# Kernel tuning notes

Hardware: AMD Instinct MI355X
Metric: run time of the kernel (lower is better)

## Reference

```python
import jax, jax.numpy as jnp
import numpy as np

B, S, H, I, E = 2, 2048, 2048, 1408, 8
TOP_K = 2


def setup_inputs() -> dict:
    key = jax.random.key(0)
    k0, k1, k2, k3, k4 = jax.random.split(key, 5)
    scale = float(np.sqrt(2.0 / (H + I)))
    return {
        "hidden_states": jax.random.normal(k0, (B, S, H), dtype=jnp.float32),
        "router_w": jax.random.normal(k1, (E, H), dtype=jnp.float32) * (H ** -0.5),
        "gate_w": jax.random.normal(k2, (E, I, H), dtype=jnp.float32) * scale,
        "up_w": jax.random.normal(k3, (E, I, H), dtype=jnp.float32) * scale,
        "down_w": jax.random.normal(k4, (E, H, I), dtype=jnp.float32) * scale,
    }


def reference(hidden_states, router_w, gate_w, up_w, down_w):
    b, s, h = hidden_states.shape
    e = router_w.shape[0]
    x = hidden_states.reshape(-1, h)  # [T, H]

    # Router: top-k logits, softmax over the selected logits.
    logits = jnp.einsum("th,eh->te", x, router_w)          # [T, E]
    top_vals, top_idx = jax.lax.top_k(logits, TOP_K)        # [T, K]
    top_w = jax.nn.softmax(top_vals, axis=-1)               # [T, K]
    # The original module only uses the top-1 expert and its weight.
    expert = top_idx[:, 0]                                  # [T] int
    weight = top_w[:, 0]                                    # [T]

    # Per-expert gated MLP applied densely, then combined with a one-hot
    # top-1 dispatch mask scaled by the routing weight (same math as the
    # gather -> grouped GEMM -> weighted scatter in the original).
    gate = jnp.einsum("th,eih->eti", x, gate_w)             # [E, T, I]
    up = jnp.einsum("th,eih->eti", x, up_w)                 # [E, T, I]
    act = jax.nn.silu(gate) * up                            # [E, T, I]
    out_e = jnp.einsum("eti,ehi->eth", act, down_w)         # [E, T, H]

    combine = jax.nn.one_hot(expert, e, dtype=x.dtype) * weight[:, None]  # [T, E]
    out = jnp.einsum("eth,te->th", out_e, combine)          # [T, H]
    return out.reshape(b, s, h)
```

## Files before the change

### kernel.cpp

```cpp
#include <hip/hip_runtime.h>
#include <stdint.h>

#define TOK 4096
#define HD 2048
#define ID 1408
#define NE 8
#define GMAX 5120
#define NTILES 40

typedef unsigned short u16;
typedef unsigned int u32;
typedef __attribute__((ext_vector_type(8))) short bf16x8;
typedef __attribute__((ext_vector_type(4))) float f32x4;

__device__ inline u16 f2bf(float f) {
  u32 u = __builtin_bit_cast(u32, f);
  u += 0x7fff + ((u >> 16) & 1);
  return (u16)(u >> 16);
}
__device__ inline u32 pk2(float a, float b) {
  return (u32)f2bf(a) | ((u32)f2bf(b) << 16);
}
__device__ inline uint4 pk8(const float4& a, const float4& b) {
  uint4 r;
  r.x = pk2(a.x, a.y); r.y = pk2(a.z, a.w);
  r.z = pk2(b.x, b.y); r.w = pk2(b.z, b.w);
  return r;
}
__device__ inline void gload_lds16(void* lds, const void* g) {
  __builtin_amdgcn_global_load_lds(
      (const __attribute__((address_space(1))) u32*)g,
      (__attribute__((address_space(3))) u32*)lds, 16, 0, 0);
}

__global__ void k_init(int* counts, int* cursors) {
  if (threadIdx.x < NE) { counts[threadIdx.x] = 0; cursors[threadIdx.x] = 0; }
}

__global__ void k_router(const float* __restrict__ x, const float* __restrict__ rw,
                         int* __restrict__ counts, int* __restrict__ expert_t,
                         float* __restrict__ weight_t) {
  const int lane = threadIdx.x & 63;
  const int t = blockIdx.x * 4 + (threadIdx.x >> 6);
  const float4* xr = (const float4*)(x + (size_t)t * HD);
  float acc[NE];
#pragma unroll
  for (int e = 0; e < NE; ++e) acc[e] = 0.f;
#pragma unroll
  for (int it = 0; it < HD / 256; ++it) {
    float4 xv = xr[it * 64 + lane];
#pragma unroll
    for (int e = 0; e < NE; ++e) {
      float4 wv = ((const float4*)(rw + e * HD))[it * 64 + lane];
      acc[e] += xv.x * wv.x + xv.y * wv.y + xv.z * wv.z + xv.w * wv.w;
    }
  }
#pragma unroll
  for (int e = 0; e < NE; ++e) {
#pragma unroll
    for (int off = 32; off > 0; off >>= 1) acc[e] += __shfl_xor(acc[e], off, 64);
  }
  if (lane == 0) {
    float v0 = -1e30f, v1 = -1e30f; int ie = 0;
#pragma unroll
    for (int e = 0; e < NE; ++e) {
      float v = acc[e];
      if (v > v0) { v1 = v0; v0 = v; ie = e; }
      else if (v > v1) { v1 = v; }
    }
    expert_t[t] = ie;
    weight_t[t] = 1.f / (1.f + __expf(v1 - v0));
    atomicAdd(counts + ie, 1);
  }
}

__global__ void k_scan(const int* __restrict__ counts, int* __restrict__ off,
                       int* __restrict__ tile_e, int* __restrict__ tile_v) {
  if (threadIdx.x != 0) return;
  int a = 0, tt = 0;
  for (int e = 0; e < NE; ++e) {
    off[e] = a;
    int c = counts[e];
    int nt = (c + 127) >> 7;
    for (int k = 0; k < nt; ++k) {
      tile_e[tt] = e;
      int v = c - (k << 7);
      tile_v[tt] = v > 128 ? 128 : v;
      ++tt;
    }
    a += nt << 7;
  }
  off[NE] = a;
  for (; tt < NTILES; ++tt) { tile_e[tt] = -1; tile_v[tt] = 0; }
}

__global__ void k_gather(const float* __restrict__ x, const int* __restrict__ expert_t,
                         const float* __restrict__ weight_t, const int* __restrict__ off,
                         int* __restrict__ cursors, int* __restrict__ rowtok,
                         float* __restrict__ wrow, u16* __restrict__ xg) {
  const int t = blockIdx.x;
  const int lane = threadIdx.x;
  const int e = expert_t[t];
  int row = 0;
  if (lane == 0) {
    int pos = atomicAdd(cursors + e, 1);
    row = off[e] + pos;
    rowtok[row] = t;
    wrow[row] = weight_t[t];
  }
  row = __shfl(row, 0, 64);
  const int r7 = row & 7;
  const float4* src = (const float4*)(x + (size_t)t * HD);
  uint4* dst = (uint4*)((char*)xg + (size_t)row * (HD * 2));
#pragma unroll
  for (int r = 0; r < 4; ++r) {
    int g = r * 64 + lane;
    float4 a = src[2 * g], b = src[2 * g + 1];
    dst[(g & ~7) | ((g & 7) ^ r7)] = pk8(a, b);
  }
}

__global__ __launch_bounds__(256, 2) void k_gateup(
    const u16* __restrict__ xg, const float* __restrict__ gate_w,
    const float* __restrict__ up_w, const int* __restrict__ tile_e,
    u16* __restrict__ act) {
  __shared__ __align__(16) char lds[49152];
  const int e = tile_e[blockIdx.y];
  if (e < 0) return;
  const int i0 = blockIdx.x * 128;
  const int m0 = blockIdx.y * 128;
  const int tid = threadIdx.x;
  const int lane = tid & 63, wv = tid >> 6;
  const int nbase = (wv >> 1) * 64, mbase = (wv & 1) * 64;
  const int l15 = lane & 15, l4 = lane >> 4;
  char* ldsA = lds;
  char* ldsG = lds + 16384;
  char* ldsU = lds + 32768;
  f32x4 accg[4][4], accu[4][4];
#pragma unroll
  for (int i = 0; i < 4; ++i)
#pragma unroll
    for (int j = 0; j < 4; ++j) {
      accg[i][j] = f32x4{0.f, 0.f, 0.f, 0.f};
      accu[i][j] = f32x4{0.f, 0.f, 0.f, 0.f};
    }
  const int trow = tid >> 1, thalf = tid & 1;
  const int wr7 = trow & 7;
  const float* gsrc = gate_w + (size_t)e * ID * HD + (size_t)(i0 + trow) * HD + thalf * 32;
  const float* usrc = up_w   + (size_t)e * ID * HD + (size_t)(i0 + trow) * HD + thalf * 32;

  for (int ks = 0; ks < HD / 64; ++ks) {
    __syncthreads();
#pragma unroll
    for (int r = 0; r < 4; ++r) {
      int o = (r * 256 + tid) * 16;
      gload_lds16(ldsA + r * 4096 + wv * 1024,
                  (const char*)xg + (size_t)(m0 + (o >> 7)) * (HD * 2) + ks * 128 + (o & 127));
    }
    {
      const float4* s = (const float4*)(gsrc + ks * 64);
      float4 v0 = s[0], v1 = s[1], v2 = s[2], v3 = s[3];
      float4 v4 = s[4], v5 = s[5], v6 = s[6], v7 = s[7];
      *(uint4*)(ldsG + trow * 128 + (((thalf * 4 + 0) ^ wr7) * 16)) = pk8(v0, v1);
      *(uint4*)(ldsG + trow * 128 + (((thalf * 4 + 1) ^ wr7) * 16)) = pk8(v2, v3);
      *(uint4*)(ldsG + trow * 128 + (((thalf * 4 + 2) ^ wr7) * 16)) = pk8(v4, v5);
      *(uint4*)(ldsG + trow * 128 + (((thalf * 4 + 3) ^ wr7) * 16)) = pk8(v6, v7);
    }
    {
      const float4* s = (const float4*)(usrc + ks * 64);
      float4 v0 = s[0], v1 = s[1], v2 = s[2], v3 = s[3];
      float4 v4 = s[4], v5 = s[5], v6 = s[6], v7 = s[7];
      *(uint4*)(ldsU + trow * 128 + (((thalf * 4 + 0) ^ wr7) * 16)) = pk8(v0, v1);
      *(uint4*)(ldsU + trow * 128 + (((thalf * 4 + 1) ^ wr7) * 16)) = pk8(v2, v3);
      *(uint4*)(ldsU + trow * 128 + (((thalf * 4 + 2) ^ wr7) * 16)) = pk8(v4, v5);
      *(uint4*)(ldsU + trow * 128 + (((thalf * 4 + 3) ^ wr7) * 16)) = pk8(v6, v7);
    }
    __syncthreads();
#pragma unroll
    for (int kk = 0; kk < 2; ++kk) {
      bf16x8 xa[4], wg[4], wu[4];
#pragma unroll
      for (int f = 0; f < 4; ++f) {
        int rx = mbase + f * 16 + l15;
        int g = kk * 4 + l4;
        xa[f] = *(const bf16x8*)(ldsA + rx * 128 + ((g ^ (rx & 7)) * 16));
        int rw_ = nbase + f * 16 + l15;
        wg[f] = *(const bf16x8*)(ldsG + rw_ * 128 + ((g ^ (rw_ & 7)) * 16));
        wu[f] = *(const bf16x8*)(ldsU + rw_ * 128 + ((g ^ (rw_ & 7)) * 16));
      }
#pragma unroll
      for (int fn = 0; fn < 4; ++fn)
#pragma unroll
        for (int fm = 0; fm < 4; ++fm) {
          accg[fn][fm] = __builtin_amdgcn_mfma_f32_16x16x32_bf16(wg[fn], xa[fm], accg[fn][fm], 0, 0, 0);
          accu[fn][fm] = __builtin_amdgcn_mfma_f32_16x16x32_bf16(wu[fn], xa[fm], accu[fn][fm], 0, 0, 0);
        }
    }
  }
#pragma unroll
  for (int fm = 0; fm < 4; ++fm) {
    int row = m0 + mbase + fm * 16 + l15;
    int r7 = row & 7;
    char* arow = (char*)act + (size_t)row * (ID * 2);
#pragma unroll
    for (int fn = 0; fn < 4; ++fn) {
      f32x4 g4 = accg[fn][fm], u4 = accu[fn][fm];
      float o0 = g4[0] / (1.f + __expf(-g4[0])) * u4[0];
      float o1 = g4[1] / (1.f + __expf(-g4[1])) * u4[1];
      float o2 = g4[2] / (1.f + __expf(-g4[2])) * u4[2];
      float o3 = g4[3] / (1.f + __expf(-g4[3])) * u4[3];
      int ig = i0 + nbase + fn * 16 + l4 * 4;
      int gi = ig >> 3;
      int pgi = (gi & ~7) | ((gi & 7) ^ r7);
      uint2 p;
      p.x = pk2(o0, o1); p.y = pk2(o2, o3);
      *(uint2*)(arow + pgi * 16 + (ig & 7) * 2) = p;
    }
  }
}

__global__ __launch_bounds__(256, 2) void k_down(
    const u16* __restrict__ act, const float* __restrict__ down_w,
    const int* __restrict__ tile_e, const int* __restrict__ tile_v,
    const int* __restrict__ rowtok, const float* __restrict__ wrow,
    float* __restrict__ out) {
  __shared__ __align__(16) char lds[32768];
  const int e = tile_e[blockIdx.y];
  if (e < 0) return;
  const int h0 = blockIdx.x * 128;
  const int m0 = blockIdx.y * 128;
  const int tid = threadIdx.x;
  const int lane = tid & 63, wv = tid >> 6;
  const int nbase = (wv >> 1) * 64, mbase = (wv & 1) * 64;
  const int l15 = lane & 15, l4 = lane >> 4;
  char* ldsA = lds;
  char* ldsW = lds + 16384;
  f32x4 acc[4][4];
#pragma unroll
  for (int i = 0; i < 4; ++i)
#pragma unroll
    for (int j = 0; j < 4; ++j) acc[i][j] = f32x4{0.f, 0.f, 0.f, 0.f};
  const int trow = tid >> 1, thalf = tid & 1;
  const int wr7 = trow & 7;
  const float* wsrc = down_w + (size_t)e * HD * ID + (size_t)(h0 + trow) * ID + thalf * 32;

  for (int ks = 0; ks < ID / 64; ++ks) {
    __syncthreads();
#pragma unroll
    for (int r = 0; r < 4; ++r) {
      int o = (r * 256 + tid) * 16;
      gload_lds16(ldsA + r * 4096 + wv * 1024,
                  (const char*)act + (size_t)(m0 + (o >> 7)) * (ID * 2) + ks * 128 + (o & 127));
    }
    {
      const float4* s = (const float4*)(wsrc + ks * 64);
      float4 v0 = s[0], v1 = s[1], v2 = s[2], v3 = s[3];
      float4 v4 = s[4], v5 = s[5], v6 = s[6], v7 = s[7];
      *(uint4*)(ldsW + trow * 128 + (((thalf * 4 + 0) ^ wr7) * 16)) = pk8(v0, v1);
      *(uint4*)(ldsW + trow * 128 + (((thalf * 4 + 1) ^ wr7) * 16)) = pk8(v2, v3);
      *(uint4*)(ldsW + trow * 128 + (((thalf * 4 + 2) ^ wr7) * 16)) = pk8(v4, v5);
      *(uint4*)(ldsW + trow * 128 + (((thalf * 4 + 3) ^ wr7) * 16)) = pk8(v6, v7);
    }
    __syncthreads();
#pragma unroll
    for (int kk = 0; kk < 2; ++kk) {
      bf16x8 xa[4], wf[4];
#pragma unroll
      for (int f = 0; f < 4; ++f) {
        int rx = mbase + f * 16 + l15;
        int g = kk * 4 + l4;
        xa[f] = *(const bf16x8*)(ldsA + rx * 128 + ((g ^ (rx & 7)) * 16));
        int rw_ = nbase + f * 16 + l15;
        wf[f] = *(const bf16x8*)(ldsW + rw_ * 128 + ((g ^ (rw_ & 7)) * 16));
      }
#pragma unroll
      for (int fn = 0; fn < 4; ++fn)
#pragma unroll
        for (int fm = 0; fm < 4; ++fm)
          acc[fn][fm] = __builtin_amdgcn_mfma_f32_16x16x32_bf16(wf[fn], xa[fm], acc[fn][fm], 0, 0, 0);
    }
  }
  const int valid = tile_v[blockIdx.y];
#pragma unroll
  for (int fm = 0; fm < 4; ++fm) {
    int ml = mbase + fm * 16 + l15;
    if (ml < valid) {
      int t = rowtok[m0 + ml];
      float wgt = wrow[m0 + ml];
      float* orow = out + (size_t)t * HD + h0 + nbase;
#pragma unroll
      for (int fn = 0; fn < 4; ++fn) {
        f32x4 v = acc[fn][fm];
        float4 o;
        o.x = v[0] * wgt; o.y = v[1] * wgt; o.z = v[2] * wgt; o.w = v[3] * wgt;
        *(float4*)(orow + fn * 16 + l4 * 4) = o;
      }
    }
  }
}

extern "C" void kernel_launch(void* const* d_in, const int* in_sizes, int n_in,
                              void* d_out, int out_size, void* d_ws, size_t ws_size,
                              hipStream_t stream) {
  const float* x  = (const float*)d_in[0];
  const float* rw = (const float*)d_in[1];
  const float* gw = (const float*)d_in[2];
  const float* uw = (const float*)d_in[3];
  const float* dw = (const float*)d_in[4];
  float* out = (float*)d_out;
  char* ws = (char*)d_ws;

  int*   counts   = (int*)(ws + 0);
  int*   cursors  = (int*)(ws + 64);
  int*   off      = (int*)(ws + 128);
  int*   tile_e   = (int*)(ws + 256);
  int*   tile_v   = (int*)(ws + 512);
  int*   expert_t = (int*)(ws + 1024);
  float* weight_t = (float*)(ws + 17408);
  int*   rowtok   = (int*)(ws + 33792);
  float* wrow     = (float*)(ws + 54272);
  u16*   xg       = (u16*)(ws + 74752);
  u16*   act      = (u16*)(ws + 74752 + (size_t)GMAX * HD * 2);

  k_init<<<1, 64, 0, stream>>>(counts, cursors);
  k_router<<<TOK / 4, 256, 0, stream>>>(x, rw, counts, expert_t, weight_t);
  k_scan<<<1, 64, 0, stream>>>(counts, off, tile_e, tile_v);
  k_gather<<<TOK, 64, 0, stream>>>(x, expert_t, weight_t, off, cursors, rowtok, wrow, xg);
  k_gateup<<<dim3(ID / 128, NTILES), 256, 0, stream>>>(xg, gw, uw, tile_e, act);
  k_down<<<dim3(HD / 128, NTILES), 256, 0, stream>>>(act, dw, tile_e, tile_v, rowtok, wrow, out);
}
```

Before: 657.1 us.

## Pre-cast expert weights to swizzled bf16 and load GEMM tiles via direct-to-LDS

Adds a cast pass that converts gate, up and down weights into a bf16 workspace copy already laid out in the LDS swizzle pattern. The GEMM kernels then fetch weight tiles with the same global_load_lds path used for activations, instead of loading fp32 per thread, packing and writing to LDS. The cost is a full read of all fp32 weights plus a bf16 write on every call, which runs for all experts rather than only per tile. It also only applies when the workspace is large enough, with the old fp32 path kept as a fallback.

```diff
diff --git a/kernel.cpp b/kernel.cpp
--- a/kernel.cpp
+++ b/kernel.cpp
@@ -8,6 +8,16 @@
 #define GMAX 5120
 #define NTILES 40
 
+#define XG_OFF   74752ULL
+#define XG_BYTES (5120ULL * 2048 * 2)
+#define ACT_OFF  (XG_OFF + XG_BYTES)
+#define ACT_BYTES (5120ULL * 1408 * 2)
+#define GWB_OFF  (ACT_OFF + ACT_BYTES)
+#define W_BYTES  (8ULL * 1408 * 2048 * 2)
+#define UWB_OFF  (GWB_OFF + W_BYTES)
+#define DWB_OFF  (UWB_OFF + W_BYTES)
+#define WS_NEED  (DWB_OFF + W_BYTES)
+
 typedef unsigned short u16;
 typedef unsigned int u32;
 typedef __attribute__((ext_vector_type(8))) short bf16x8;
@@ -35,6 +45,18 @@
 
 __global__ void k_init(int* counts, int* cursors) {
   if (threadIdx.x < NE) { counts[threadIdx.x] = 0; cursors[threadIdx.x] = 0; }
+}
+
+__global__ void k_cast(const float* __restrict__ src, u16* __restrict__ dst, int K) {
+  const int row = blockIdx.x;
+  const int g = threadIdx.x;
+  const int ng = K >> 3;
+  if (g < ng) {
+    const float4* s = (const float4*)(src + (size_t)row * K + g * 8);
+    float4 a = s[0], b = s[1];
+    uint4* d = (uint4*)((char*)dst + (size_t)row * K * 2);
+    d[(g & ~7) | ((g & 7) ^ (row & 7))] = pk8(a, b);
+  }
 }
 
 __global__ void k_router(const float* __restrict__ x, const float* __restrict__ rw,
@@ -120,7 +142,162 @@
   }
 }
 
-__global__ __launch_bounds__(256, 2) void k_gateup(
+__global__ __launch_bounds__(256, 2) void k_gateup_b(
+    const u16* __restrict__ xg, const u16* __restrict__ gwb,
+    const u16* __restrict__ uwb, const int* __restrict__ tile_e,
+    u16* __restrict__ act) {
+  __shared__ __align__(16) char lds[49152];
+  const int e = tile_e[blockIdx.y];
+  if (e < 0) return;
+  const int i0 = blockIdx.x * 128;
+  const int m0 = blockIdx.y * 128;
+  const int tid = threadIdx.x;
+  const int lane = tid & 63, wv = tid >> 6;
+  const int nbase = (wv >> 1) * 64, mbase = (wv & 1) * 64;
+  const int l15 = lane & 15, l4 = lane >> 4;
+  char* ldsA = lds;
+  char* ldsG = lds + 16384;
+  char* ldsU = lds + 32768;
+  f32x4 accg[4][4], accu[4][4];
+#pragma unroll
+  for (int i = 0; i < 4; ++i)
+#pragma unroll
+    for (int j = 0; j < 4; ++j) {
+      accg[i][j] = f32x4{0.f, 0.f, 0.f, 0.f};
+      accu[i][j] = f32x4{0.f, 0.f, 0.f, 0.f};
+    }
+  const char* asrc = (const char*)xg  + (size_t)m0 * (HD * 2);
+  const char* gsrc = (const char*)gwb + (size_t)(e * ID + i0) * (HD * 2);
+  const char* usrc = (const char*)uwb + (size_t)(e * ID + i0) * (HD * 2);
+
+  for (int ks = 0; ks < HD / 64; ++ks) {
+    __syncthreads();
+#pragma unroll
+    for (int r = 0; r < 4; ++r) {
+      int o = (r * 256 + tid) * 16;
+      size_t rowoff = (size_t)(o >> 7) * (HD * 2) + ks * 128 + (o & 127);
+      char* ldst = lds + r * 4096 + wv * 1024;
+      gload_lds16(ldst,           asrc + rowoff);
+      gload_lds16(ldst + 16384,   gsrc + rowoff);
+      gload_lds16(ldst + 32768,   usrc + rowoff);
+    }
+    __syncthreads();
+#pragma unroll
+    for (int kk = 0; kk < 2; ++kk) {
+      bf16x8 xa[4], wg[4], wu[4];
+#pragma unroll
+      for (int f = 0; f < 4; ++f) {
+        int rx = mbase + f * 16 + l15;
+        int g = kk * 4 + l4;
+        xa[f] = *(const bf16x8*)(ldsA + rx * 128 + ((g ^ (rx & 7)) * 16));
+        int rw_ = nbase + f * 16 + l15;
+        wg[f] = *(const bf16x8*)(ldsG + rw_ * 128 + ((g ^ (rw_ & 7)) * 16));
+        wu[f] = *(const bf16x8*)(ldsU + rw_ * 128 + ((g ^ (rw_ & 7)) * 16));
+      }
+#pragma unroll
+      for (int fn = 0; fn < 4; ++fn)
+#pragma unroll
+        for (int fm = 0; fm < 4; ++fm) {
+          accg[fn][fm] = __builtin_amdgcn_mfma_f32_16x16x32_bf16(wg[fn], xa[fm], accg[fn][fm], 0, 0, 0);
+          accu[fn][fm] = __builtin_amdgcn_mfma_f32_16x16x32_bf16(wu[fn], xa[fm], accu[fn][fm], 0, 0, 0);
+        }
+    }
+  }
+#pragma unroll
+  for (int fm = 0; fm < 4; ++fm) {
+    int row = m0 + mbase + fm * 16 + l15;
+    int r7 = row & 7;
+    char* arow = (char*)act + (size_t)row * (ID * 2);
+#pragma unroll
+    for (int fn = 0; fn < 4; ++fn) {
+      f32x4 g4 = accg[fn][fm], u4 = accu[fn][fm];
+      float o0 = g4[0] / (1.f + __expf(-g4[0])) * u4[0];
+      float o1 = g4[1] / (1.f + __expf(-g4[1])) * u4[1];
+      float o2 = g4[2] / (1.f + __expf(-g4[2])) * u4[2];
+      float o3 = g4[3] / (1.f + __expf(-g4[3])) * u4[3];
+      int ig = i0 + nbase + fn * 16 + l4 * 4;
+      int gi = ig >> 3;
+      int pgi = (gi & ~7) | ((gi & 7) ^ r7);
+      uint2 p;
+      p.x = pk2(o0, o1); p.y = pk2(o2, o3);
+      *(uint2*)(arow + pgi * 16 + (ig & 7) * 2) = p;
+    }
+  }
+}
+
+__global__ __launch_bounds__(256, 2) void k_down_b(
+    const u16* __restrict__ act, const u16* __restrict__ dwb,
+    const int* __restrict__ tile_e, const int* __restrict__ tile_v,
+    const int* __restrict__ rowtok, const float* __restrict__ wrow,
+    float* __restrict__ out) {
+  __shared__ __align__(16) char lds[32768];
+  const int e = tile_e[blockIdx.y];
+  if (e < 0) return;
+  const int h0 = blockIdx.x * 128;
+  const int m0 = blockIdx.y * 128;
+  const int tid = threadIdx.x;
+  const int lane = tid & 63, wv = tid >> 6;
+  const int nbase = (wv >> 1) * 64, mbase = (wv & 1) * 64;
+  const int l15 = lane & 15, l4 = lane >> 4;
+  char* ldsA = lds;
+  char* ldsW = lds + 16384;
+  f32x4 acc[4][4];
+#pragma unroll
+  for (int i = 0; i < 4; ++i)
+#pragma unroll
+    for (int j = 0; j < 4; ++j) acc[i][j] = f32x4{0.f, 0.f, 0.f, 0.f};
+  const char* asrc = (const char*)act + (size_t)m0 * (ID * 2);
+  const char* wsrc = (const char*)dwb + (size_t)(e * HD + h0) * (ID * 2);
+
+  for (int ks = 0; ks < ID / 64; ++ks) {
+    __syncthreads();
+#pragma unroll
+    for (int r = 0; r < 4; ++r) {
+      int o = (r * 256 + tid) * 16;
+      size_t rowoff = (size_t)(o >> 7) * (ID * 2) + ks * 128 + (o & 127);
+      char* ldst = lds + r * 4096 + wv * 1024;
+      gload_lds16(ldst,         asrc + rowoff);
+      gload_lds16(ldst + 16384, wsrc + rowoff);
+    }
+    __syncthreads();
+#pragma unroll
+    for (int kk = 0; kk < 2; ++kk) {
+      bf16x8 xa[4], wf[4];
+#pragma unroll
+      for (int f = 0; f < 4; ++f) {
+        int rx = mbase + f * 16 + l15;
+        int g = kk * 4 + l4;
+        xa[f] = *(const bf16x8*)(ldsA + rx * 128 + ((g ^ (rx & 7)) * 16));
+        int rw_ = nbase + f * 16 + l15;
+        wf[f] = *(const bf16x8*)(ldsW + rw_ * 128 + ((g ^ (rw_ & 7)) * 16));
+      }
+#pragma unroll
+      for (int fn = 0; fn < 4; ++fn)
+#pragma unroll
+        for (int fm = 0; fm < 4; ++fm)
+          acc[fn][fm] = __builtin_amdgcn_mfma_f32_16x16x32_bf16(wf[fn], xa[fm], acc[fn][fm], 0, 0, 0);
+    }
+  }
+  const int valid = tile_v[blockIdx.y];
+#pragma unroll
+  for (int fm = 0; fm < 4; ++fm) {
+    int ml = mbase + fm * 16 + l15;
+    if (ml < valid) {
+      int t = rowtok[m0 + ml];
+      float wgt = wrow[m0 + ml];
+      float* orow = out + (size_t)t * HD + h0 + nbase;
+#pragma unroll
+      for (int fn = 0; fn < 4; ++fn) {
+        f32x4 v = acc[fn][fm];
+        float4 o;
+        o.x = v[0] * wgt; o.y = v[1] * wgt; o.z = v[2] * wgt; o.w = v[3] * wgt;
+        *(float4*)(orow + fn * 16 + l4 * 4) = o;
+      }
+    }
+  }
+}
+
+__global__ __launch_bounds__(256, 2) void k_gateup_f(
     const u16* __restrict__ xg, const float* __restrict__ gate_w,
     const float* __restrict__ up_w, const int* __restrict__ tile_e,
     u16* __restrict__ act) {
@@ -148,7 +325,6 @@
   const int wr7 = trow & 7;
   const float* gsrc = gate_w + (size_t)e * ID * HD + (size_t)(i0 + trow) * HD + thalf * 32;
   const float* usrc = up_w   + (size_t)e * ID * HD + (size_t)(i0 + trow) * HD + thalf * 32;
-
   for (int ks = 0; ks < HD / 64; ++ks) {
     __syncthreads();
 #pragma unroll
@@ -219,7 +395,7 @@
   }
 }
 
-__global__ __launch_bounds__(256, 2) void k_down(
+__global__ __launch_bounds__(256, 2) void k_down_f(
     const u16* __restrict__ act, const float* __restrict__ down_w,
     const int* __restrict__ tile_e, const int* __restrict__ tile_v,
     const int* __restrict__ rowtok, const float* __restrict__ wrow,
@@ -243,7 +419,6 @@
   const int trow = tid >> 1, thalf = tid & 1;
   const int wr7 = trow & 7;
   const float* wsrc = down_w + (size_t)e * HD * ID + (size_t)(h0 + trow) * ID + thalf * 32;
-
   for (int ks = 0; ks < ID / 64; ++ks) {
     __syncthreads();
 #pragma unroll
@@ -319,13 +494,28 @@
   float* weight_t = (float*)(ws + 17408);
   int*   rowtok   = (int*)(ws + 33792);
   float* wrow     = (float*)(ws + 54272);
-  u16*   xg       = (u16*)(ws + 74752);
-  u16*   act      = (u16*)(ws + 74752 + (size_t)GMAX * HD * 2);
+  u16*   xg       = (u16*)(ws + XG_OFF);
+  u16*   act      = (u16*)(ws + ACT_OFF);
+  u16*   gwb      = (u16*)(ws + GWB_OFF);
+  u16*   uwb      = (u16*)(ws + UWB_OFF);
+  u16*   dwb      = (u16*)(ws + DWB_OFF);
+
+  const bool big = ws_size >= WS_NEED;
 
   k_init<<<1, 64, 0, stream>>>(counts, cursors);
+  if (big) {
+    k_cast<<<NE * ID, 256, 0, stream>>>(gw, gwb, HD);
+    k_cast<<<NE * ID, 256, 0, stream>>>(uw, uwb, HD);
+    k_cast<<<NE * HD, 256, 0, stream>>>(dw, dwb, ID);
+  }
   k_router<<<TOK / 4, 256, 0, stream>>>(x, rw, counts, expert_t, weight_t);
   k_scan<<<1, 64, 0, stream>>>(counts, off, tile_e, tile_v);
   k_gather<<<TOK, 64, 0, stream>>>(x, expert_t, weight_t, off, cursors, rowtok, wrow, xg);
-  k_gateup<<<dim3(ID / 128, NTILES), 256, 0, stream>>>(xg, gw, uw, tile_e, act);
-  k_down<<<dim3(HD / 128, NTILES), 256, 0, stream>>>(act, dw, tile_e, tile_v, rowtok, wrow, out);
-}
+  if (big) {
+    k_gateup_b<<<dim3(ID / 128, NTILES), 256, 0, stream>>>(xg, gwb, uwb, tile_e, act);
+    k_down_b<<<dim3(HD / 128, NTILES), 256, 0, stream>>>(act, dwb, tile_e, tile_v, rowtok, wrow, out);
+  } else {
+    k_gateup_f<<<dim3(ID / 128, NTILES), 256, 0, stream>>>(xg, gw, uw, tile_e, act);
+    k_down_f<<<dim3(HD / 128, NTILES), 256, 0, stream>>>(act, dw, tile_e, tile_v, rowtok, wrow, out);
+  }
+}
```

New measurement: 527.6 us. 1.25x faster.
